# Optimization experiments

Hardware: AMD Instinct MI355X
Metric: run time of the kernel (lower is better)

## Reference

```python
import jax, jax.numpy as jnp
import numpy as np

K_TOP = 128
NORM_TYPE = 'l2'  # 'l2' | 'l1' | 'avg'

def _norm(x, norm_type):
    if norm_type == 'l2':
        return jnp.sum(jnp.square(x), axis=2)
    if norm_type == 'l1':
        return jnp.sum(jnp.abs(x), axis=2)
    return jnp.sum(x, axis=2)  # 'avg'

def setup_inputs() -> dict:
    key = jax.random.key(0)
    x = jax.random.normal(key, (64, 8192, 256), dtype=jnp.float32)
    return {"x": x}

def reference(x) -> jnp.ndarray:
    # x: [B, N, D]
    norms = _norm(x, NORM_TYPE)                      # [B, N]
    _, idx = jax.lax.top_k(norms, K_TOP)             # [B, k], descending-norm order
    # gather the k selected embedding rows per batch element -> [B, k, D]
    return jnp.take_along_axis(x, idx[:, :, None], axis=1)
```

## Files before the change

kernel.cpp:

```cpp
#include <hip/hip_runtime.h>

constexpr int B = 64;
constexpr int N = 8192;
constexpr int D = 256;
constexpr int K = 128;
constexpr int CHUNKS = 32;
constexpr int RPC = N / CHUNKS;
constexpr int NCAND = CHUNKS * K;
constexpr int TILE = 64;

typedef unsigned long long ull;

__device__ __forceinline__ int bitrev6(int l) {
    return ((l & 1) << 5) | ((l & 2) << 3) | ((l & 4) << 1)
         | ((l & 8) >> 1) | ((l & 16) >> 3) | ((l & 32) >> 5);
}

__global__ __launch_bounds__(256) void norm_select_kernel(const float* __restrict__ x,
                                                          ull* __restrict__ cand) {
    __shared__ float part[TILE][65];
    __shared__ ull skeys[RPC];
    const int bid   = blockIdx.x;
    const int batch = bid >> 5;
    const int chunk = bid & (CHUNKS - 1);
    const int tid   = threadIdx.x;
    const int w     = tid >> 6;
    const int lane  = tid & 63;
    const int brl   = bitrev6(lane);
    const size_t rowbase = (size_t)batch * N + (size_t)chunk * RPC;

    for (int tile = 0; tile < 4; ++tile) {
        const int r0 = w * 16;
        const float* wbase = x + (rowbase + (size_t)(tile * TILE + r0)) * D;
        #pragma unroll
        for (int it0 = 0; it0 < 16; it0 += 4) {
            float4 v[4];
            #pragma unroll
            for (int u = 0; u < 4; ++u)
                v[u] = reinterpret_cast<const float4*>(wbase + (size_t)(it0 + u) * D)[lane];
            #pragma unroll
            for (int u = 0; u < 4; ++u)
                part[r0 + it0 + u][brl] = v[u].x * v[u].x + v[u].y * v[u].y
                                        + v[u].z * v[u].z + v[u].w * v[u].w;
        }
        __syncthreads();

        if (tid < TILE) {
            float q[8];
            float g[8];
            #pragma unroll
            for (int grp = 0; grp < 8; ++grp) {
                #pragma unroll
                for (int j = 0; j < 8; ++j) q[j] = part[tid][grp * 8 + j];
                g[grp] = ((q[0] + q[1]) + (q[2] + q[3]))
                       + ((q[4] + q[5]) + (q[6] + q[7]));
            }
            const float s = ((g[0] + g[1]) + (g[2] + g[3]))
                          + ((g[4] + g[5]) + (g[6] + g[7]));
            const int grow = chunk * RPC + tile * TILE + tid;
            skeys[tile * TILE + tid] = ((ull)__float_as_uint(s) << 32)
                                     | (unsigned int)(N - 1 - grow);
        }
        __syncthreads();
    }

    const ull mine = skeys[tid];
    int rank = 0;
    for (int j = 0; j < RPC; ++j)
        rank += (skeys[j] > mine) ? 1 : 0;
    if (rank < K)
        cand[(size_t)bid * K + rank] = mine;
}

__global__ __launch_bounds__(1024) void topk_gather_kernel(const ull* __restrict__ cand_in,
                                                           const float* __restrict__ x,
                                                           float* __restrict__ out) {
    __shared__ ull keys[NCAND];
    __shared__ unsigned int hist[256];
    __shared__ unsigned int seg[32];
    __shared__ ull s_prefix;
    __shared__ unsigned int s_krem;
    __shared__ int s_done;
    __shared__ unsigned int s_cnt;
    __shared__ ull sel[K];
    __shared__ int sorted_src[K];

    const int b    = blockIdx.x;
    const int tid  = threadIdx.x;
    const int lane = tid & 63;

    for (int i = tid; i < NCAND; i += 1024)
        keys[i] = cand_in[(size_t)b * NCAND + i];
    if (tid == 0) { s_prefix = 0ull; s_krem = K; s_done = 0; s_cnt = 0u; }
    __syncthreads();

    for (int p = 7; p >= 0; --p) {
        if (s_done) break;
        const int shift = p * 8;
        const ull          prefix = s_prefix;
        const unsigned int krem   = s_krem;
        if (tid < 256) hist[tid] = 0u;
        __syncthreads();

        if (p == 7) {
            for (int i = tid; i < NCAND; i += 1024) {
                const unsigned int d = (unsigned int)(keys[i] >> 56);
                ull rem = __ballot(true);
                while (rem) {
                    const int leader = __ffsll(rem) - 1;
                    const unsigned int dl = __shfl(d, leader, 64);
                    const ull grp = __ballot(d == dl);
                    if (lane == leader) atomicAdd(&hist[dl], (unsigned int)__popcll(grp));
                    rem &= ~grp;
                }
            }
        } else {
            for (int i = tid; i < NCAND; i += 1024) {
                const ull key = keys[i];
                if ((key >> (shift + 8)) == (prefix >> (shift + 8)))
                    atomicAdd(&hist[(unsigned int)(key >> shift) & 255u], 1u);
            }
        }
        __syncthreads();

        if (tid < 32) {
            unsigned int s = 0;
            #pragma unroll
            for (int d2 = 0; d2 < 8; ++d2) s += hist[tid * 8 + d2];
            seg[tid] = s;
        }
        __syncthreads();

        if (tid < 256) {
            unsigned int cnt_gt = 0;
            const int hiSeg = (tid >> 3) + 1;
            for (int s2 = hiSeg; s2 < 32; ++s2) cnt_gt += seg[s2];
            for (int d2 = tid + 1; d2 < hiSeg * 8; ++d2) cnt_gt += hist[d2];
            const unsigned int h = hist[tid];
            if (cnt_gt < krem && krem <= cnt_gt + h) {
                s_prefix = prefix | ((ull)tid << shift);
                s_krem   = krem - cnt_gt;
                if (h == krem - cnt_gt) s_done = 1;
            }
        }
        __syncthreads();
    }

    const ull T = s_prefix;
    for (int i = tid; i < NCAND; i += 1024) {
        const ull key = keys[i];
        if (key >= T) {
            const unsigned int pos = atomicAdd(&s_cnt, 1u);
            sel[pos] = key;
        }
    }
    __syncthreads();

    if (tid < K) {
        const ull key = sel[tid];
        int rank = 0;
        for (int j = 0; j < K; ++j) rank += (sel[j] > key) ? 1 : 0;
        sorted_src[rank] = N - 1 - (int)(key & 0xFFFFFFFFu);
    }
    __syncthreads();

    for (int r = tid >> 6; r < K; r += 16) {
        const int src = sorted_src[r];
        const float4 v = reinterpret_cast<const float4*>(x + ((size_t)b * N + src) * D)[lane];
        reinterpret_cast<float4*>(out + ((size_t)b * K + r) * D)[lane] = v;
    }
}

extern "C" void kernel_launch(void* const* d_in, const int* in_sizes, int n_in,
                              void* d_out, int out_size, void* d_ws, size_t ws_size,
                              hipStream_t stream) {
    const float* x = (const float*)d_in[0];
    float* out = (float*)d_out;
    ull* cand = (ull*)d_ws;

    norm_select_kernel<<<B * CHUNKS, 256, 0, stream>>>(x, cand);
    topk_gather_kernel<<<B, 1024, 0, stream>>>(cand, x, out);
}
```

Measured before the change: 116.4 us.

## Remove block barriers from norm pass and split gather into separate wide kernel

In the norm kernel, each wavefront now owns 64 contiguous rows and reduces its own partials with vectorized LDS reads. This removes the per-tile block-wide __syncthreads and the single-wave reduction bottleneck. The top-k kernel now writes only sorted indices, and a new gather kernel spread over many blocks copies the rows, so the gather is no longer limited to 64 blocks. This costs an extra kernel launch and an index round trip through global memory.

```diff
diff --git a/kernel.cpp b/kernel.cpp
--- a/kernel.cpp
+++ b/kernel.cpp
@@ -7,7 +7,6 @@
 constexpr int CHUNKS = 32;
 constexpr int RPC = N / CHUNKS;
 constexpr int NCAND = CHUNKS * K;
-constexpr int TILE = 64;
 
 typedef unsigned long long ull;
 
@@ -18,7 +17,7 @@
 
 __global__ __launch_bounds__(256) void norm_select_kernel(const float* __restrict__ x,
                                                           ull* __restrict__ cand) {
-    __shared__ float part[TILE][65];
+    __shared__ __attribute__((aligned(16))) float part[4][16][68];
     __shared__ ull skeys[RPC];
     const int bid   = blockIdx.x;
     const int batch = bid >> 5;
@@ -28,41 +27,40 @@
     const int lane  = tid & 63;
     const int brl   = bitrev6(lane);
     const size_t rowbase = (size_t)batch * N + (size_t)chunk * RPC;
+    const float* wbase = x + (rowbase + (size_t)w * 64) * D;
 
-    for (int tile = 0; tile < 4; ++tile) {
-        const int r0 = w * 16;
-        const float* wbase = x + (rowbase + (size_t)(tile * TILE + r0)) * D;
+    for (int g = 0; g < 4; ++g) {
         #pragma unroll
         for (int it0 = 0; it0 < 16; it0 += 4) {
             float4 v[4];
             #pragma unroll
             for (int u = 0; u < 4; ++u)
-                v[u] = reinterpret_cast<const float4*>(wbase + (size_t)(it0 + u) * D)[lane];
+                v[u] = reinterpret_cast<const float4*>(
+                           wbase + (size_t)(g * 16 + it0 + u) * D)[lane];
             #pragma unroll
             for (int u = 0; u < 4; ++u)
-                part[r0 + it0 + u][brl] = v[u].x * v[u].x + v[u].y * v[u].y
-                                        + v[u].z * v[u].z + v[u].w * v[u].w;
+                part[w][it0 + u][brl] = v[u].x * v[u].x + v[u].y * v[u].y
+                                      + v[u].z * v[u].z + v[u].w * v[u].w;
         }
-        __syncthreads();
-
-        if (tid < TILE) {
-            float q[8];
-            float g[8];
+        if (lane < 16) {
+            const float4* rowp = reinterpret_cast<const float4*>(&part[w][lane][0]);
+            float gg[8];
             #pragma unroll
             for (int grp = 0; grp < 8; ++grp) {
-                #pragma unroll
-                for (int j = 0; j < 8; ++j) q[j] = part[tid][grp * 8 + j];
-                g[grp] = ((q[0] + q[1]) + (q[2] + q[3]))
-                       + ((q[4] + q[5]) + (q[6] + q[7]));
+                const float4 qa = rowp[grp * 2];
+                const float4 qb = rowp[grp * 2 + 1];
+                gg[grp] = ((qa.x + qa.y) + (qa.z + qa.w))
+                        + ((qb.x + qb.y) + (qb.z + qb.w));
             }
-            const float s = ((g[0] + g[1]) + (g[2] + g[3]))
-                          + ((g[4] + g[5]) + (g[6] + g[7]));
-            const int grow = chunk * RPC + tile * TILE + tid;
-            skeys[tile * TILE + tid] = ((ull)__float_as_uint(s) << 32)
-                                     | (unsigned int)(N - 1 - grow);
+            const float s = ((gg[0] + gg[1]) + (gg[2] + gg[3]))
+                          + ((gg[4] + gg[5]) + (gg[6] + gg[7]));
+            const int lrow = w * 64 + g * 16 + lane;
+            const int grow = chunk * RPC + lrow;
+            skeys[lrow] = ((ull)__float_as_uint(s) << 32)
+                        | (unsigned int)(N - 1 - grow);
         }
-        __syncthreads();
     }
+    __syncthreads();
 
     const ull mine = skeys[tid];
     int rank = 0;
@@ -72,9 +70,8 @@
         cand[(size_t)bid * K + rank] = mine;
 }
 
-__global__ __launch_bounds__(1024) void topk_gather_kernel(const ull* __restrict__ cand_in,
-                                                           const float* __restrict__ x,
-                                                           float* __restrict__ out) {
+__global__ __launch_bounds__(1024) void topk_select_kernel(const ull* __restrict__ cand_in,
+                                                           int* __restrict__ idx_out) {
     __shared__ ull keys[NCAND];
     __shared__ unsigned int hist[256];
     __shared__ unsigned int seg[32];
@@ -83,7 +80,6 @@
     __shared__ int s_done;
     __shared__ unsigned int s_cnt;
     __shared__ ull sel[K];
-    __shared__ int sorted_src[K];
 
     const int b    = blockIdx.x;
     const int tid  = threadIdx.x;
@@ -160,15 +156,19 @@
         const ull key = sel[tid];
         int rank = 0;
         for (int j = 0; j < K; ++j) rank += (sel[j] > key) ? 1 : 0;
-        sorted_src[rank] = N - 1 - (int)(key & 0xFFFFFFFFu);
+        idx_out[b * K + rank] = N - 1 - (int)(key & 0xFFFFFFFFu);
     }
-    __syncthreads();
+}
 
-    for (int r = tid >> 6; r < K; r += 16) {
-        const int src = sorted_src[r];
-        const float4 v = reinterpret_cast<const float4*>(x + ((size_t)b * N + src) * D)[lane];
-        reinterpret_cast<float4*>(out + ((size_t)b * K + r) * D)[lane] = v;
-    }
+__global__ __launch_bounds__(256) void gather_kernel(const float* __restrict__ x,
+                                                     const int* __restrict__ idx,
+                                                     float* __restrict__ out) {
+    const int row  = blockIdx.x * 4 + (threadIdx.x >> 6);
+    const int lane = threadIdx.x & 63;
+    const int b    = row >> 7;
+    const int src  = idx[row];
+    const float4 v = reinterpret_cast<const float4*>(x + ((size_t)b * N + src) * D)[lane];
+    reinterpret_cast<float4*>(out + (size_t)row * D)[lane] = v;
 }
 
 extern "C" void kernel_launch(void* const* d_in, const int* in_sizes, int n_in,
@@ -177,7 +177,9 @@
     const float* x = (const float*)d_in[0];
     float* out = (float*)d_out;
     ull* cand = (ull*)d_ws;
+    int* idx  = (int*)(cand + (size_t)B * NCAND);
 
     norm_select_kernel<<<B * CHUNKS, 256, 0, stream>>>(x, cand);
-    topk_gather_kernel<<<B, 1024, 0, stream>>>(cand, x, out);
+    topk_select_kernel<<<B, 1024, 0, stream>>>(cand, idx);
+    gather_kernel<<<B * K / 4, 256, 0, stream>>>(x, idx, out);
 }
```

Result: slower. 121.0 us (+4.0%).
